# Kernel optimization log

Measured on AMD Instinct MI355X. Metric: run time of the kernel, lower is better.

## Reference

```python
import jax, jax.numpy as jnp
import numpy as np
import math

# ---- model constants (match init_kwargs) ----
B, T, HID = 2, 4096, 2048
H, D = 16, 128            # heads, head_dim; num_kv_heads == H
ROPE_DIM = 64             # head_dim * partial_rotary_factor (0.5)
THETA = 10000.0
EPS = 1e-6
CHUNK = 64                # chunk size for the chunked simple-GLA scan
LAYER_IDX, N_LAYERS = 12, 32


def _alibi_slopes(n):
    # power-of-2 path of build_slope_tensor
    start = 2.0 ** (-(2.0 ** -(math.log2(n) - 3.0)))
    return np.array([start ** (i + 1) for i in range(n)], dtype=np.float32)


def _layer_slope():
    scale = 1.0 - (LAYER_IDX - 1) / (N_LAYERS - 1) + 1e-5
    return jnp.asarray(-_alibi_slopes(H) * scale)  # [H], negative log-decay per step


def _rmsnorm(x, w):
    xf = x.astype(jnp.float32)
    var = jnp.mean(xf * xf, axis=-1, keepdims=True)
    return (w * (xf * jax.lax.rsqrt(var + EPS)).astype(x.dtype))


def _group_rmsnorm(x, w, groups):
    # x: [..., groups*gd]; normalize within each group, then elementwise weight
    shp = x.shape
    xg = x.reshape(shp[:-1] + (groups, shp[-1] // groups)).astype(jnp.float32)
    var = jnp.mean(xg * xg, axis=-1, keepdims=True)
    xn = (xg * jax.lax.rsqrt(var + EPS)).astype(x.dtype).reshape(shp)
    return w * xn


def _rope_cos_sin(position_ids):
    inv_freq = 1.0 / (THETA ** (jnp.arange(0, ROPE_DIM, 2, dtype=jnp.float32) / ROPE_DIM))
    freqs = position_ids.astype(jnp.float32)[..., None] * inv_freq  # [B,T,ROPE_DIM/2]
    emb = jnp.concatenate([freqs, freqs], axis=-1)                  # [B,T,ROPE_DIM]
    return jnp.cos(emb), jnp.sin(emb)


def _rotate_half(x):
    x1, x2 = jnp.split(x, 2, axis=-1)
    return jnp.concatenate([-x2, x1], axis=-1)


def _apply_rope(x, cos, sin):
    # x: [B,T,H,D]; partial rotary on first ROPE_DIM dims
    c = cos[:, :, None, :]
    s = sin[:, :, None, :]
    x_rot, x_pass = x[..., :ROPE_DIM], x[..., ROPE_DIM:]
    x_rot = x_rot * c + _rotate_half(x_rot) * s
    return jnp.concatenate([x_rot, x_pass], axis=-1)


def _chunk_simple_gla(q, k, v, slope):
    # q,k,v: [B,T,H,D]; slope: [H] (negative per-step log-decay)
    # recurrence: S_t = exp(slope)*S_{t-1} + k_t^T v_t ; o_t = q_t S_t
    q = q * (D ** -0.5)
    nc = T // CHUNK
    def to_chunks(x):
        # [B,T,H,D] -> [nc,B,H,CHUNK,D]
        return x.reshape(B, nc, CHUNK, H, D).transpose(1, 0, 3, 2, 4)
    qc, kc, vc = to_chunks(q), to_chunks(k), to_chunks(v)

    i = jnp.arange(CHUNK, dtype=jnp.float32)
    g = slope[:, None, None]                                  # [H,1,1]
    mask = jnp.where(i[:, None] >= i[None, :],
                     jnp.exp(g * (i[:, None] - i[None, :])), 0.0)   # [H,C,C]
    q_dec = jnp.exp(slope[:, None] * (i + 1.0))               # [H,C]
    k_dec = jnp.exp(slope[:, None] * (CHUNK - 1.0 - i))       # [H,C]
    ch_dec = jnp.exp(slope * CHUNK)                           # [H]

    S0 = jnp.zeros((B, H, D, D), q.dtype)

    def step(S, inp):
        qi, ki, vi = inp                                       # [B,H,C,D]
        att = jnp.einsum('bhcd,bhed->bhce', qi, ki) * mask[None]
        intra = jnp.einsum('bhce,bhed->bhcd', att, vi)
        inter = jnp.einsum('bhcd,bhde->bhce', qi * q_dec[None, :, :, None], S)
        S_new = ch_dec[None, :, None, None] * S + \
            jnp.einsum('bhcd,bhce->bhde', ki * k_dec[None, :, :, None], vi)
        return S_new, intra + inter

    _, o = jax.lax.scan(step, S0, (qc, kc, vc))                # o: [nc,B,H,C,D]
    return o.transpose(1, 0, 3, 2, 4).reshape(B, T, H * D)


def setup_inputs() -> dict:
    key = jax.random.key(0)
    ks = jax.random.split(key, 4)
    return {
        'hidden_states': jax.random.normal(ks[0], (B, T, HID), jnp.float32),
        'w_qkv': jax.random.normal(ks[1], (3 * H * D, HID), jnp.float32) * 0.02,
        'q_ln_w': jnp.ones((D,), jnp.float32),
        'k_ln_w': jnp.ones((D,), jnp.float32),
        'g_norm_w': jnp.ones((H * D,), jnp.float32),
        'w_g_proj': jax.random.normal(ks[2], (H * D, HID), jnp.float32) * 0.02,
        'w_dense': jax.random.normal(ks[3], (HID, H * D), jnp.float32) * 0.02,
        'position_ids': jnp.arange(B * T, dtype=jnp.int32).reshape(B, T) % T,
    }


def reference(hidden_states, w_qkv, q_ln_w, k_ln_w, g_norm_w, w_g_proj, w_dense, position_ids):
    slope = _layer_slope()
    qkv = jnp.einsum('bth,oh->bto', hidden_states, w_qkv)
    q, k, v = jnp.split(qkv, [H * D, 2 * H * D], axis=-1)
    q = q.reshape(B, T, H, D)
    k = k.reshape(B, T, H, D)
    v = v.reshape(B, T, H, D)
    # qk-norm (per-head RMSNorm)
    q = _rmsnorm(q, q_ln_w)
    k = _rmsnorm(k, k_ln_w)
    # partial RoPE
    cos, sin = _rope_cos_sin(position_ids)
    q = _apply_rope(q, cos, sin)
    k = _apply_rope(k, cos, sin)
    # chunked lightning (simple-GLA) linear attention
    o = _chunk_simple_gla(q, k, v, slope)                      # [B,T,H*D]
    # group RMSNorm (per head) + sigmoid output gate, then output proj
    gate = jax.nn.sigmoid(jnp.einsum('bth,oh->bto', hidden_states, w_g_proj))
    o = _group_rmsnorm(o, g_norm_w, groups=H) * gate
    return jnp.einsum('bto,ho->bth', o, w_dense)
```

## Files before the change

### kernel.cpp

```cpp
#include <hip/hip_runtime.h>
#include <math.h>

typedef short bf16x8 __attribute__((ext_vector_type(8)));
typedef float f32x4 __attribute__((ext_vector_type(4)));

#define LOG2E 1.4426950408889634f
#define GSCALE 0.6451712903225806f

__device__ __forceinline__ float bf2f(unsigned short h) {
    union { unsigned u; float f; } v; v.u = ((unsigned)h) << 16; return v.f;
}
__device__ __forceinline__ unsigned short f2bf(float f) {
    union { float f; unsigned u; } v; v.f = f;
    unsigned r = v.u + 0x7FFFu + ((v.u >> 16) & 1u);
    return (unsigned short)(r >> 16);
}

#define GLD16(lds, g)                                                          \
    __builtin_amdgcn_global_load_lds(                                          \
        (const __attribute__((address_space(1))) void*)(g),                    \
        (__attribute__((address_space(3))) void*)(lds), 16, 0, 0)

#define MFMA16(a, b, c) __builtin_amdgcn_mfma_f32_16x16x32_bf16(a, b, c, 0, 0, 0)

__device__ __forceinline__ void dsr128(bf16x8& d, const unsigned short* p) {
    unsigned off = (unsigned)(unsigned long long)
        (const __attribute__((address_space(3))) unsigned short*)p;
    asm volatile("ds_read_b128 %0, %1" : "=v"(d) : "v"(off));
}

struct us4 { unsigned short a, b, c, d; };
__global__ __launch_bounds__(256) void cvt4_f32_bf16(
    const float* __restrict__ s0, const float* __restrict__ s1,
    const float* __restrict__ s2, const float* __restrict__ s3,
    unsigned short* __restrict__ dst, int c0, int c1, int c2, int n4)
{
    int i = blockIdx.x * 256 + threadIdx.x;
    if (i >= n4) return;
    const float* s; int off;
    if (i < c0)      { s = s0; off = i; }
    else if (i < c1) { s = s1; off = i - c0; }
    else if (i < c2) { s = s2; off = i - c1; }
    else             { s = s3; off = i - c2; }
    float4 v = ((const float4*)s)[off];
    us4 o = { f2bf(v.x), f2bf(v.y), f2bf(v.z), f2bf(v.w) };
    ((us4*)dst)[i] = o;
}

template <int EPI>
__global__ __launch_bounds__(512, 2) void gemm256(
    const unsigned short* __restrict__ A, const unsigned short* __restrict__ Bt,
    void* __restrict__ Cv,
    unsigned short* __restrict__ Qp, unsigned short* __restrict__ Kp,
    unsigned short* __restrict__ Vp, unsigned short* __restrict__ Gb,
    int M, int N, int K)
{
    __shared__ __attribute__((aligned(16))) unsigned short lA[2][16384];
    __shared__ __attribute__((aligned(16))) unsigned short lB[2][16384];

    const int tid  = threadIdx.x;
    const int lane = tid & 63, wave = tid >> 6;
    const int quad = lane >> 4, lr = lane & 15;
    const int wm   = (wave >> 2) * 128;
    const int wn   = (wave & 3) * 64;
    const int lsw  = lr & 7;

    const int lin = (int)(blockIdx.y * gridDim.x + blockIdx.x);
    const int xcd = lin & 7, j = lin >> 3;
    const int RPC = (int)gridDim.y >> 3;
    const int bm  = xcd * RPC + (j % RPC);
    const int bn  = j / RPC;

    const unsigned short* Ab = A  + (long long)bm * 256 * K;
    const unsigned short* Bb = Bt + (long long)bn * 256 * K;

    const int r0 = tid >> 3, g0 = tid & 7;
    const long long gbase = (long long)r0 * K + ((g0 ^ (r0 & 7)) * 8);
    const int lbase = tid * 8;

#define STAGE4(lds, gb, kt)                                                    \
    _Pragma("unroll") for (int w = 0; w < 4; ++w)                              \
        GLD16((lds) + w * 4096 + lbase,                                        \
              (gb) + (long long)w * 64 * K + (kt) + gbase);

    f32x4 acc[8][4] = {};
    bf16x8 a0[8], b0[4], a1[8], b1[4];

#define LDA8A(F, buf, s)                                                       \
    _Pragma("unroll") for (int i = 0; i < 8; ++i)                              \
        dsr128(F[i], (buf) + (wm + i * 16 + lr) * 64 +                         \
                     ((((s) * 4 + quad) ^ lsw) * 8));
#define LDB4A(F, buf, s)                                                       \
    _Pragma("unroll") for (int j2 = 0; j2 < 4; ++j2)                           \
        dsr128(F[j2], (buf) + (wn + j2 * 16 + lr) * 64 +                       \
                      ((((s) * 4 + quad) ^ lsw) * 8));
#define MFMAS(FA, FB)                                                          \
    _Pragma("unroll") for (int i = 0; i < 8; ++i)                              \
    _Pragma("unroll") for (int j2 = 0; j2 < 4; ++j2)                           \
        acc[i][j2] = MFMA16(FA[i], FB[j2], acc[i][j2]);

#define BARR()   asm volatile("s_barrier" ::: "memory")
#define LGKM0()  asm volatile("s_waitcnt lgkmcnt(0)" ::: "memory")
#define LGKM12() asm volatile("s_waitcnt lgkmcnt(12)" ::: "memory")
#define VM8()    asm volatile("s_waitcnt vmcnt(8)" ::: "memory")
#define SBAR()   __builtin_amdgcn_sched_barrier(0)
#define MCLUST(FA, FB)                                                         \
    do { SBAR(); __builtin_amdgcn_s_setprio(1); MFMAS(FA, FB);                 \
         __builtin_amdgcn_s_setprio(0); SBAR(); } while (0)

    STAGE4(lA[0], Ab, 0);  STAGE4(lB[0], Bb, 0);
    STAGE4(lA[1], Ab, 64); STAGE4(lB[1], Bb, 64);
    VM8();
    BARR();
    LDA8A(a0, lA[0], 0); LDB4A(b0, lB[0], 0);

    const int NT = K >> 6;
    for (int it = 0; it < (NT >> 1); ++it) {
        const int knu = (2 * it + 2 < NT) ? (2 * it + 2) * 64 : 0;
        const int knv = (2 * it + 3 < NT) ? (2 * it + 3) * 64 : 0;
        LDA8A(a1, lA[0], 1); LDB4A(b1, lB[0], 1);
        LGKM12();
        MCLUST(a0, b0);
        LGKM0(); BARR();
        STAGE4(lA[0], Ab, knu); STAGE4(lB[0], Bb, knu);
        VM8(); BARR();
        LDA8A(a0, lA[1], 0); LDB4A(b0, lB[1], 0);
        LGKM12();
        MCLUST(a1, b1);
        LDA8A(a1, lA[1], 1); LDB4A(b1, lB[1], 1);
        LGKM12();
        MCLUST(a0, b0);
        LGKM0(); BARR();
        STAGE4(lA[1], Ab, knv); STAGE4(lB[1], Bb, knv);
        VM8(); BARR();
        LDA8A(a0, lA[0], 0); LDB4A(b0, lB[0], 0);
        LGKM12();
        MCLUST(a1, b1);
    }
    asm volatile("s_waitcnt vmcnt(0) lgkmcnt(0)" ::: "memory");

#pragma unroll
    for (int i = 0; i < 8; ++i)
#pragma unroll
        for (int j2 = 0; j2 < 4; ++j2)
#pragma unroll
            for (int r = 0; r < 4; ++r) {
                int row = bm * 256 + wm + i * 16 + quad * 4 + r;
                int col = bn * 256 + wn + j2 * 16 + lr;
                float vv = acc[i][j2][r];
                if (EPI == 0) {
                    if (col < 6144) {
                        int tens = col >> 11, h = (col >> 7) & 15, e = col & 127;
                        int b = row >> 12, t = row & 4095;
                        long long dst = (((long long)(b * 16 + h)) * 4096 + t) * 128 + e;
                        unsigned short* P = (tens == 0) ? Qp : ((tens == 1) ? Kp : Vp);
                        P[dst] = f2bf(vv);
                    } else {
                        vv = 1.0f / (1.0f + __expf(-vv));
                        Gb[(long long)row * 2048 + (col - 6144)] = f2bf(vv);
                    }
                } else {
                    ((float*)Cv)[(long long)row * N + col] = vv;
                }
            }
#undef STAGE4
#undef LDA8A
#undef LDB4A
#undef MFMAS
#undef BARR
#undef LGKM0
#undef LGKM12
#undef VM8
#undef SBAR
#undef MCLUST
}

__global__ __launch_bounds__(256) void norm_rope(
    unsigned short* __restrict__ Qp, unsigned short* __restrict__ Kp,
    const float* __restrict__ qw, const float* __restrict__ kw,
    const int* __restrict__ pos_ids)
{
    const int bid  = blockIdx.x;
    const int tg   = bid & 1023, h = (bid >> 10) & 15, b = bid >> 14;
    const int wave = threadIdx.x >> 6, lane = threadIdx.x & 63;
    const int t    = tg * 4 + wave;
    const long long rowbase = (((long long)(b * 16 + h)) * 4096 + t) * 128;
    const int pos = pos_ids[b * 4096 + t];
    const int d0  = lane * 2;

    float c0 = 1.f, s0 = 0.f, c1 = 1.f, s1 = 0.f;
    if (lane < 32) {
        float fj0 = (float)(d0 & 31), fj1 = (float)((d0 + 1) & 31);
        float if0 = exp2f(-fj0 * 0.4152410118609203f);
        float if1 = exp2f(-fj1 * 0.4152410118609203f);
        sincosf((float)pos * if0, &s0, &c0);
        sincosf((float)pos * if1, &s1, &c1);
    }
    const float w0q = qw[d0], w1q = qw[d0 + 1];
    const float w0k = kw[d0], w1k = kw[d0 + 1];

#pragma unroll
    for (int which = 0; which < 2; ++which) {
        unsigned short* P = which ? Kp : Qp;
        float w0 = which ? w0k : w0q, w1 = which ? w1k : w1q;
        unsigned u = *(const unsigned*)(P + rowbase + d0);
        float x0 = bf2f(u & 0xFFFF), x1 = bf2f(u >> 16);
        float ss = x0 * x0 + x1 * x1;
#pragma unroll
        for (int off = 32; off; off >>= 1) ss += __shfl_xor(ss, off);
        float r  = rsqrtf(ss * (1.0f / 128.0f) + 1e-6f);
        float xn0 = x0 * r * w0;
        float xn1 = x1 * r * w1;
        float p0 = __shfl_xor(xn0, 16);
        float p1 = __shfl_xor(xn1, 16);
        float y0, y1;
        if (d0 < 32)      { y0 = xn0 * c0 - p0 * s0; y1 = xn1 * c1 - p1 * s1; }
        else if (d0 < 64) { y0 = xn0 * c0 + p0 * s0; y1 = xn1 * c1 + p1 * s1; }
        else              { y0 = xn0; y1 = xn1; }
        if (which == 0) { y0 *= 0.08838834764831845f; y1 *= 0.08838834764831845f; }
        *(unsigned*)(P + rowbase + d0) =
            (unsigned)f2bf(y0) | ((unsigned)f2bf(y1) << 16);
    }
}

__global__ __launch_bounds__(256) void gla_chunk(
    const unsigned short* __restrict__ Qp, const unsigned short* __restrict__ Kp,
    const unsigned short* __restrict__ Vp,
    unsigned short* __restrict__ Oint, unsigned short* __restrict__ Ubuf)
{
    __shared__ __attribute__((aligned(16))) unsigned short sK[64 * 136];
    __shared__ __attribute__((aligned(16))) unsigned short sVT[128 * 72];
    __shared__ __attribute__((aligned(16))) unsigned short sKT[128 * 72];
    __shared__ __attribute__((aligned(16))) unsigned short sAtt[64 * 72];

    const int bid = blockIdx.x;
    const int n = bid & 63, h = (bid >> 6) & 15, b = bid >> 10;
    const int tid = threadIdx.x, wave = tid >> 6, lane = tid & 63;
    const int quad = lane >> 4, lr = lane & 15;
    const float gl2 = -exp2f(-0.5f * (float)(h + 1)) * GSCALE * LOG2E;

    const long long rb = (((long long)(b * 16 + h)) * 4096 + (long long)n * 64) * 128;

    const int cS = wave * 16 + lr;
    const float qsc = exp2f(gl2 * (float)cS);
    bf16x8 qf[4];
#pragma unroll
    for (int ks = 0; ks < 4; ++ks) {
        union { uint4 v; unsigned short s[8]; } in, ou;
        in.v = *(const uint4*)(Qp + rb + cS * 128 + ks * 32 + quad * 8);
#pragma unroll
        for (int j = 0; j < 8; ++j) ou.s[j] = f2bf(bf2f(in.s[j]) * qsc);
        qf[ks] = *(bf16x8*)&ou;
    }
#pragma unroll
    for (int rr = 0; rr < 4; ++rr) {
        int idx = rr * 256 + tid;
        int c = idx >> 4, d8 = (idx & 15) << 3;
        *(uint4*)(sK + c * 136 + d8) = *(const uint4*)(Kp + rb + c * 128 + d8);
    }
#pragma unroll
    for (int rr = 0; rr < 4; ++rr) {
        int idx = rr * 256 + tid;
        int c = idx & 63, g8 = (idx >> 6) << 3;
        union { uint4 v; unsigned short s[8]; } vv, kk;
        vv.v = *(const uint4*)(Vp + rb + c * 128 + g8);
        kk.v = *(const uint4*)(Kp + rb + c * 128 + g8);
        float kdsc = exp2f(gl2 * (float)(64 - c));
#pragma unroll
        for (int j = 0; j < 8; ++j) {
            sVT[(g8 + j) * 72 + c] = vv.s[j];
            sKT[(g8 + j) * 72 + c] = f2bf(bf2f(kk.s[j]) * kdsc);
        }
    }
    __syncthreads();

    f32x4 aacc[4] = {};
#pragma unroll
    for (int nj = 0; nj < 4; ++nj)
#pragma unroll
        for (int ks = 0; ks < 4; ++ks) {
            bf16x8 bf = *(const bf16x8*)(sK + (nj * 16 + lr) * 136 + ks * 32 + quad * 8);
            aacc[nj] = MFMA16(qf[ks], bf, aacc[nj]);
        }
#pragma unroll
    for (int nj = 0; nj < 4; ++nj) {
        int c2 = nj * 16 + lr;
        float colf = exp2f(-gl2 * (float)c2);
#pragma unroll
        for (int r = 0; r < 4; ++r) {
            int c = wave * 16 + quad * 4 + r;
            sAtt[c * 72 + c2] = f2bf((c >= c2) ? aacc[nj][r] * colf : 0.0f);
        }
    }
    f32x4 Sacc[2][8] = {};
#pragma unroll
    for (int me = 0; me < 2; ++me)
#pragma unroll
        for (int ks = 0; ks < 2; ++ks) {
            bf16x8 af = *(const bf16x8*)(sVT + (wave * 32 + me * 16 + lr) * 72 + ks * 32 + quad * 8);
#pragma unroll
            for (int dj = 0; dj < 8; ++dj) {
                bf16x8 bf = *(const bf16x8*)(sKT + (dj * 16 + lr) * 72 + ks * 32 + quad * 8);
                Sacc[me][dj] = MFMA16(af, bf, Sacc[me][dj]);
            }
        }
    const long long ub = ((long long)((b * 16 + h) * 64 + n)) * 16384;
#pragma unroll
    for (int me = 0; me < 2; ++me)
#pragma unroll
        for (int r = 0; r < 4; ++r) {
            int e = wave * 32 + me * 16 + quad * 4 + r;
#pragma unroll
            for (int dj = 0; dj < 8; ++dj)
                Ubuf[ub + e * 128 + dj * 16 + lr] = f2bf(Sacc[me][dj][r]);
        }
    __syncthreads();

    f32x4 oacc[8] = {};
#pragma unroll
    for (int ks = 0; ks < 2; ++ks) {
        bf16x8 af = *(const bf16x8*)(sAtt + cS * 72 + ks * 32 + quad * 8);
#pragma unroll
        for (int ej = 0; ej < 8; ++ej) {
            bf16x8 bf = *(const bf16x8*)(sVT + (ej * 16 + lr) * 72 + ks * 32 + quad * 8);
            oacc[ej] = MFMA16(af, bf, oacc[ej]);
        }
    }
#pragma unroll
    for (int ej = 0; ej < 8; ++ej)
#pragma unroll
        for (int r = 0; r < 4; ++r) {
            int c = wave * 16 + quad * 4 + r;
            long long off = ((long long)(b * 4096 + n * 64 + c)) * 2048 + h * 128 + ej * 16 + lr;
            Oint[off] = f2bf(oacc[ej][r]);
        }
}

__global__ __launch_bounds__(256) void gla_scan(
    const unsigned short* __restrict__ Ubuf, unsigned short* __restrict__ STbuf)
{
    const int bid = blockIdx.x;
    const int es = bid & 7, bh = bid >> 3;
    const int h = bh & 15;
    const float gl2 = -exp2f(-0.5f * (float)(h + 1)) * GSCALE * LOG2E;
    const float chd = exp2f(gl2 * 64.0f);
    const int tid = threadIdx.x;
    const long long base = (long long)bh * 64 * 16384 + es * 2048 + tid * 8;
    float st[8] = {};
    for (int n = 0; n < 64; ++n) {
        long long a = base + (long long)n * 16384;
        union { uint4 v; unsigned short s[8]; } u, o;
        u.v = *(const uint4*)(Ubuf + a);
#pragma unroll
        for (int j = 0; j < 8; ++j) o.s[j] = f2bf(st[j]);
        *(uint4*)(STbuf + a) = o.v;
#pragma unroll
        for (int j = 0; j < 8; ++j) st[j] = st[j] * chd + bf2f(u.s[j]);
    }
}

__global__ __launch_bounds__(256) void gla_inter(
    const unsigned short* __restrict__ Qp, const unsigned short* __restrict__ STbuf,
    unsigned short* __restrict__ Ob, const unsigned short* __restrict__ Gb,
    const float* __restrict__ W)
{
    __shared__ __attribute__((aligned(16))) unsigned short sST[128 * 136];
    const int bid = blockIdx.x;
    const int n = bid & 63, h = (bid >> 6) & 15, b = bid >> 10;
    const int tid = threadIdx.x, wave = tid >> 6, lane = tid & 63;
    const int quad = lane >> 4, lr = lane & 15;
    const float gl2 = -exp2f(-0.5f * (float)(h + 1)) * GSCALE * LOG2E;
    const long long rb = (((long long)(b * 16 + h)) * 4096 + (long long)n * 64) * 128;
    const long long stb = ((long long)((b * 16 + h) * 64 + n)) * 16384;

#pragma unroll
    for (int rr = 0; rr < 8; ++rr) {
        int idx = rr * 256 + tid;
        int row = idx >> 4, d8 = (idx & 15) << 3;
        *(uint4*)(sST + row * 136 + d8) = *(const uint4*)(STbuf + stb + row * 128 + d8);
    }
    const int cS = wave * 16 + lr;
    const float qsc = exp2f(gl2 * (float)cS);
    bf16x8 qf[4];
#pragma unroll
    for (int ks = 0; ks < 4; ++ks) {
        union { uint4 v; unsigned short s[8]; } in, ou;
        in.v = *(const uint4*)(Qp + rb + cS * 128 + ks * 32 + quad * 8);
#pragma unroll
        for (int j = 0; j < 8; ++j) ou.s[j] = f2bf(bf2f(in.s[j]) * qsc);
        qf[ks] = *(bf16x8*)&ou;
    }
    __syncthreads();

    f32x4 oacc[8] = {};
#pragma unroll
    for (int ks = 0; ks < 4; ++ks)
#pragma unroll
        for (int ej = 0; ej < 8; ++ej) {
            bf16x8 bf = *(const bf16x8*)(sST + (ej * 16 + lr) * 136 + ks * 32 + quad * 8);
            oacc[ej] = MFMA16(qf[ks], bf, oacc[ej]);
        }

    float w[8];
#pragma unroll
    for (int ej = 0; ej < 8; ++ej) w[ej] = W[h * 128 + ej * 16 + lr];

    float ss[4] = {};
#pragma unroll
    for (int r = 0; r < 4; ++r) {
        int c = wave * 16 + quad * 4 + r;
        long long off = ((long long)(b * 4096 + n * 64 + c)) * 2048 + h * 128;
#pragma unroll
        for (int ej = 0; ej < 8; ++ej) {
            float v = oacc[ej][r] + bf2f(Ob[off + ej * 16 + lr]);
            oacc[ej][r] = v;
            ss[r] += v * v;
        }
    }
#pragma unroll
    for (int r = 0; r < 4; ++r) {
#pragma unroll
        for (int o2 = 1; o2 < 16; o2 <<= 1) ss[r] += __shfl_xor(ss[r], o2);
        float rn = rsqrtf(ss[r] * (1.0f / 128.0f) + 1e-6f);
        int c = wave * 16 + quad * 4 + r;
        long long off = ((long long)(b * 4096 + n * 64 + c)) * 2048 + h * 128;
#pragma unroll
        for (int ej = 0; ej < 8; ++ej) {
            float g = bf2f(Gb[off + ej * 16 + lr]);
            Ob[off + ej * 16 + lr] = f2bf(oacc[ej][r] * rn * w[ej] * g);
        }
    }
}

extern "C" void kernel_launch(void* const* d_in, const int* in_sizes, int n_in,
                              void* d_out, int out_size, void* d_ws, size_t ws_size,
                              hipStream_t stream)
{
    const float* hid   = (const float*)d_in[0];
    const float* w_qkv = (const float*)d_in[1];
    const float* q_ln  = (const float*)d_in[2];
    const float* k_ln  = (const float*)d_in[3];
    const float* g_nw  = (const float*)d_in[4];
    const float* w_g   = (const float*)d_in[5];
    const float* w_d   = (const float*)d_in[6];
    const int*   pos   = (const int*)d_in[7];

    const size_t PLANE = (size_t)2 * 16 * 4096 * 128;
    unsigned short* Qp    = (unsigned short*)d_ws;
    unsigned short* Kp    = Qp + PLANE;
    unsigned short* Vp    = Kp + PLANE;
    unsigned short* Ob    = Vp + PLANE;
    unsigned short* Gb    = Ob + PLANE;
    unsigned short* hidb  = Gb + PLANE;
    unsigned short* wqkvb = hidb + (size_t)8192 * 2048;
    unsigned short* wgb   = wqkvb + (size_t)6144 * 2048;
    unsigned short* wdb   = wgb + (size_t)2048 * 2048;
    unsigned short* Ubuf  = hidb;
    unsigned short* STbuf = Kp;

    dim3 blk(256);
    const int c0 = 8192 * 2048 / 4;
    const int c1 = c0 + 6144 * 2048 / 4;
    const int c2 = c1 + 2048 * 2048 / 4;
    const int n4 = c2 + 2048 * 2048 / 4;
    cvt4_f32_bf16<<<(n4 + 255) / 256, blk, 0, stream>>>(
        hid, w_qkv, w_g, w_d, hidb, c0, c1, c2, n4);

    gemm256<0><<<dim3(32, 32), dim3(512), 0, stream>>>(
        hidb, wqkvb, nullptr, Qp, Kp, Vp, Gb, 8192, 8192, 2048);
    norm_rope<<<32768, blk, 0, stream>>>(Qp, Kp, q_ln, k_ln, pos);
    gla_chunk<<<2048, blk, 0, stream>>>(Qp, Kp, Vp, Ob, Ubuf);
    gla_scan<<<256, blk, 0, stream>>>(Ubuf, STbuf);
    gla_inter<<<2048, blk, 0, stream>>>(Qp, STbuf, Ob, Gb, g_nw);
    gemm256<2><<<dim3(8, 32), dim3(512), 0, stream>>>(
        Ob, wdb, d_out, nullptr, nullptr, nullptr, nullptr, 8192, 2048, 2048);
}
```

Baseline: 610.7 us.

## Fuse QK RMSNorm and partial RoPE into QKV GEMM epilogue

```diff
diff --git a/kernel.cpp b/kernel.cpp
--- a/kernel.cpp
+++ b/kernel.cpp
@@ -53,6 +53,8 @@
     void* __restrict__ Cv,
     unsigned short* __restrict__ Qp, unsigned short* __restrict__ Kp,
     unsigned short* __restrict__ Vp, unsigned short* __restrict__ Gb,
+    const float* __restrict__ qwp, const float* __restrict__ kwp,
+    const int* __restrict__ posp,
     int M, int N, int K)
 {
     __shared__ __attribute__((aligned(16))) unsigned short lA[2][16384];
@@ -101,7 +103,6 @@
 
 #define BARR()   asm volatile("s_barrier" ::: "memory")
 #define LGKM0()  asm volatile("s_waitcnt lgkmcnt(0)" ::: "memory")
-#define LGKM12() asm volatile("s_waitcnt lgkmcnt(12)" ::: "memory")
 #define VM8()    asm volatile("s_waitcnt vmcnt(8)" ::: "memory")
 #define SBAR()   __builtin_amdgcn_sched_barrier(0)
 #define MCLUST(FA, FB)                                                         \
@@ -113,114 +114,138 @@
     VM8();
     BARR();
     LDA8A(a0, lA[0], 0); LDB4A(b0, lB[0], 0);
+    LGKM0();
 
     const int NT = K >> 6;
-    for (int it = 0; it < (NT >> 1); ++it) {
-        const int knu = (2 * it + 2 < NT) ? (2 * it + 2) * 64 : 0;
-        const int knv = (2 * it + 3 < NT) ? (2 * it + 3) * 64 : 0;
-        LDA8A(a1, lA[0], 1); LDB4A(b1, lB[0], 1);
-        LGKM12();
+    for (int t = 0; t < NT; ++t) {
+        unsigned short* cA = lA[t & 1];
+        unsigned short* cB = lB[t & 1];
+        unsigned short* oA = lA[(t & 1) ^ 1];
+        unsigned short* oB = lB[(t & 1) ^ 1];
+        const int kn = (t + 2 < NT) ? (t + 2) * 64 : 0;
+        LDA8A(a1, cA, 1); LDB4A(b1, cB, 1);
         MCLUST(a0, b0);
         LGKM0(); BARR();
-        STAGE4(lA[0], Ab, knu); STAGE4(lB[0], Bb, knu);
+        STAGE4(cA, Ab, kn); STAGE4(cB, Bb, kn);
         VM8(); BARR();
-        LDA8A(a0, lA[1], 0); LDB4A(b0, lB[1], 0);
-        LGKM12();
+        LDA8A(a0, oA, 0); LDB4A(b0, oB, 0);
         MCLUST(a1, b1);
-        LDA8A(a1, lA[1], 1); LDB4A(b1, lB[1], 1);
-        LGKM12();
-        MCLUST(a0, b0);
-        LGKM0(); BARR();
-        STAGE4(lA[1], Ab, knv); STAGE4(lB[1], Bb, knv);
-        VM8(); BARR();
-        LDA8A(a0, lA[0], 0); LDB4A(b0, lB[0], 0);
-        LGKM12();
-        MCLUST(a1, b1);
+        LGKM0();
     }
     asm volatile("s_waitcnt vmcnt(0) lgkmcnt(0)" ::: "memory");
 
-#pragma unroll
-    for (int i = 0; i < 8; ++i)
-#pragma unroll
-        for (int j2 = 0; j2 < 4; ++j2)
-#pragma unroll
-            for (int r = 0; r < 4; ++r) {
-                int row = bm * 256 + wm + i * 16 + quad * 4 + r;
-                int col = bn * 256 + wn + j2 * 16 + lr;
-                float vv = acc[i][j2][r];
-                if (EPI == 0) {
-                    if (col < 6144) {
-                        int tens = col >> 11, h = (col >> 7) & 15, e = col & 127;
-                        int b = row >> 12, t = row & 4095;
-                        long long dst = (((long long)(b * 16 + h)) * 4096 + t) * 128 + e;
-                        unsigned short* P = (tens == 0) ? Qp : ((tens == 1) ? Kp : Vp);
-                        P[dst] = f2bf(vv);
+    if (EPI == 0) {
+        const int tens = bn >> 3;
+        if (tens < 2) {
+            BARR();
+            float* red = (float*)&lA[0][0];
+#pragma unroll
+            for (int i = 0; i < 8; ++i)
+#pragma unroll
+                for (int r = 0; r < 4; ++r) {
+                    float s = 0.f;
+#pragma unroll
+                    for (int j2 = 0; j2 < 4; ++j2) {
+                        float x = acc[i][j2][r]; s += x * x;
+                    }
+#pragma unroll
+                    for (int o = 1; o < 16; o <<= 1) s += __shfl_xor(s, o);
+                    if (lr == 0) red[wave * 128 + i * 16 + quad * 4 + r] = s;
+                }
+            BARR();
+            const float* Wv = tens ? kwp : qwp;
+            float wreg[4];
+#pragma unroll
+            for (int j2 = 0; j2 < 4; ++j2)
+                wreg[j2] = Wv[((wave & 1) << 6) + j2 * 16 + lr];
+            const float qmul = tens ? 1.0f : 0.08838834764831845f;
+            const bool dorope = ((wave & 1) == 0);
+            float f0 = 0.f, f1 = 0.f;
+            if (dorope) {
+                f0 = exp2f(-(float)lr        * 0.4152410118609203f);
+                f1 = exp2f(-(float)(16 + lr) * 0.4152410118609203f);
+            }
+            unsigned short* P = tens ? Kp : Qp;
+            const int hh = (2 * bn + ((wave >> 1) & 1)) & 15;
+#pragma unroll
+            for (int i = 0; i < 8; ++i)
+#pragma unroll
+                for (int r = 0; r < 4; ++r) {
+                    int row = bm * 256 + wm + i * 16 + quad * 4 + r;
+                    int idx = i * 16 + quad * 4 + r;
+                    float tot = red[wave * 128 + idx] + red[(wave ^ 1) * 128 + idx];
+                    float rms = rsqrtf(tot * (1.0f / 128.0f) + 1e-6f);
+                    float xh[4], y[4];
+#pragma unroll
+                    for (int j2 = 0; j2 < 4; ++j2)
+                        xh[j2] = acc[i][j2][r] * rms * wreg[j2];
+                    if (dorope) {
+                        int pos = posp[row];
+                        float sn0, cs0, sn1, cs1;
+                        sincosf((float)pos * f0, &sn0, &cs0);
+                        sincosf((float)pos * f1, &sn1, &cs1);
+                        y[0] = xh[0] * cs0 - xh[2] * sn0;
+                        y[2] = xh[2] * cs0 + xh[0] * sn0;
+                        y[1] = xh[1] * cs1 - xh[3] * sn1;
+                        y[3] = xh[3] * cs1 + xh[1] * sn1;
                     } else {
-                        vv = 1.0f / (1.0f + __expf(-vv));
+                        y[0] = xh[0]; y[1] = xh[1]; y[2] = xh[2]; y[3] = xh[3];
+                    }
+                    int b = row >> 12, t2 = row & 4095;
+                    long long dstb = (((long long)(b * 16 + hh)) * 4096 + t2) * 128
+                                     + ((wave & 1) << 6) + lr;
+#pragma unroll
+                    for (int j2 = 0; j2 < 4; ++j2)
+                        P[dstb + j2 * 16] = f2bf(y[j2] * qmul);
+                }
+        } else if (tens == 2) {
+#pragma unroll
+            for (int i = 0; i < 8; ++i)
+#pragma unroll
+                for (int j2 = 0; j2 < 4; ++j2)
+#pragma unroll
+                    for (int r = 0; r < 4; ++r) {
+                        int row = bm * 256 + wm + i * 16 + quad * 4 + r;
+                        int col = bn * 256 + wn + j2 * 16 + lr;
+                        int h = (col >> 7) & 15, e = col & 127;
+                        int b = row >> 12, t2 = row & 4095;
+                        long long dst = (((long long)(b * 16 + h)) * 4096 + t2) * 128 + e;
+                        Vp[dst] = f2bf(acc[i][j2][r]);
+                    }
+        } else {
+#pragma unroll
+            for (int i = 0; i < 8; ++i)
+#pragma unroll
+                for (int j2 = 0; j2 < 4; ++j2)
+#pragma unroll
+                    for (int r = 0; r < 4; ++r) {
+                        int row = bm * 256 + wm + i * 16 + quad * 4 + r;
+                        int col = bn * 256 + wn + j2 * 16 + lr;
+                        float vv = 1.0f / (1.0f + __expf(-acc[i][j2][r]));
                         Gb[(long long)row * 2048 + (col - 6144)] = f2bf(vv);
                     }
-                } else {
-                    ((float*)Cv)[(long long)row * N + col] = vv;
+        }
+    } else {
+#pragma unroll
+        for (int i = 0; i < 8; ++i)
+#pragma unroll
+            for (int j2 = 0; j2 < 4; ++j2)
+#pragma unroll
+                for (int r = 0; r < 4; ++r) {
+                    int row = bm * 256 + wm + i * 16 + quad * 4 + r;
+                    int col = bn * 256 + wn + j2 * 16 + lr;
+                    ((float*)Cv)[(long long)row * N + col] = acc[i][j2][r];
                 }
-            }
+    }
 #undef STAGE4
 #undef LDA8A
 #undef LDB4A
 #undef MFMAS
 #undef BARR
 #undef LGKM0
-#undef LGKM12
 #undef VM8
 #undef SBAR
 #undef MCLUST
-}
-
-__global__ __launch_bounds__(256) void norm_rope(
-    unsigned short* __restrict__ Qp, unsigned short* __restrict__ Kp,
-    const float* __restrict__ qw, const float* __restrict__ kw,
-    const int* __restrict__ pos_ids)
-{
-    const int bid  = blockIdx.x;
-    const int tg   = bid & 1023, h = (bid >> 10) & 15, b = bid >> 14;
-    const int wave = threadIdx.x >> 6, lane = threadIdx.x & 63;
-    const int t    = tg * 4 + wave;
-    const long long rowbase = (((long long)(b * 16 + h)) * 4096 + t) * 128;
-    const int pos = pos_ids[b * 4096 + t];
-    const int d0  = lane * 2;
-
-    float c0 = 1.f, s0 = 0.f, c1 = 1.f, s1 = 0.f;
-    if (lane < 32) {
-        float fj0 = (float)(d0 & 31), fj1 = (float)((d0 + 1) & 31);
-        float if0 = exp2f(-fj0 * 0.4152410118609203f);
-        float if1 = exp2f(-fj1 * 0.4152410118609203f);
-        sincosf((float)pos * if0, &s0, &c0);
-        sincosf((float)pos * if1, &s1, &c1);
-    }
-    const float w0q = qw[d0], w1q = qw[d0 + 1];
-    const float w0k = kw[d0], w1k = kw[d0 + 1];
-
-#pragma unroll
-    for (int which = 0; which < 2; ++which) {
-        unsigned short* P = which ? Kp : Qp;
-        float w0 = which ? w0k : w0q, w1 = which ? w1k : w1q;
-        unsigned u = *(const unsigned*)(P + rowbase + d0);
-        float x0 = bf2f(u & 0xFFFF), x1 = bf2f(u >> 16);
-        float ss = x0 * x0 + x1 * x1;
-#pragma unroll
-        for (int off = 32; off; off >>= 1) ss += __shfl_xor(ss, off);
-        float r  = rsqrtf(ss * (1.0f / 128.0f) + 1e-6f);
-        float xn0 = x0 * r * w0;
-        float xn1 = x1 * r * w1;
-        float p0 = __shfl_xor(xn0, 16);
-        float p1 = __shfl_xor(xn1, 16);
-        float y0, y1;
-        if (d0 < 32)      { y0 = xn0 * c0 - p0 * s0; y1 = xn1 * c1 - p1 * s1; }
-        else if (d0 < 64) { y0 = xn0 * c0 + p0 * s0; y1 = xn1 * c1 + p1 * s1; }
-        else              { y0 = xn0; y1 = xn1; }
-        if (which == 0) { y0 *= 0.08838834764831845f; y1 *= 0.08838834764831845f; }
-        *(unsigned*)(P + rowbase + d0) =
-            (unsigned)f2bf(y0) | ((unsigned)f2bf(y1) << 16);
-    }
 }
 
 __global__ __launch_bounds__(256) void gla_chunk(
@@ -467,11 +492,12 @@
         hid, w_qkv, w_g, w_d, hidb, c0, c1, c2, n4);
 
     gemm256<0><<<dim3(32, 32), dim3(512), 0, stream>>>(
-        hidb, wqkvb, nullptr, Qp, Kp, Vp, Gb, 8192, 8192, 2048);
-    norm_rope<<<32768, blk, 0, stream>>>(Qp, Kp, q_ln, k_ln, pos);
+        hidb, wqkvb, nullptr, Qp, Kp, Vp, Gb, q_ln, k_ln, pos,
+        8192, 8192, 2048);
     gla_chunk<<<2048, blk, 0, stream>>>(Qp, Kp, Vp, Ob, Ubuf);
     gla_scan<<<256, blk, 0, stream>>>(Ubuf, STbuf);
     gla_inter<<<2048, blk, 0, stream>>>(Qp, STbuf, Ob, Gb, g_nw);
     gemm256<2><<<dim3(8, 32), dim3(512), 0, stream>>>(
-        Ob, wdb, d_out, nullptr, nullptr, nullptr, nullptr, 8192, 2048, 2048);
-}
+        Ob, wdb, d_out, nullptr, nullptr, nullptr, nullptr,
+        nullptr, nullptr, nullptr, 8192, 2048, 2048);
+}
```

Result: slower. 629.3 us (+3.0%).
